# Kernel optimization log

Hardware: AMD Instinct MI355X
Metric: run time of the kernel (lower is better)

Reference implementation:

```python
import jax, jax.numpy as jnp
import numpy as np
from jax import lax

D_MODEL = 64      # feature_dim
D_STATE = 16      # state_dim
D_CONV = 4        # conv_dim
EXPAND = 2
D_INNER = EXPAND * D_MODEL          # 128
DT_RANK = (D_MODEL + 15) // 16      # ceil(d_model/16) = 4, mamba default
IN_DIM = 64
LN_EPS = 1e-3                        # keras LayerNormalization default epsilon


def setup_inputs() -> dict:
    key = jax.random.key(0)
    ks = jax.random.split(key, 12)
    B, L = 16, 8192
    s = 0.02
    x = jax.random.normal(ks[0], (B, L, IN_DIM), jnp.float32)
    W_in = jax.random.normal(ks[1], (IN_DIM, D_MODEL), jnp.float32) * s
    b_in = jnp.zeros((D_MODEL,), jnp.float32)
    in_proj_w = jax.random.normal(ks[2], (D_MODEL, 2 * D_INNER), jnp.float32) * s
    conv_w = jax.random.normal(ks[3], (D_INNER, D_CONV), jnp.float32) * 0.1
    conv_b = jnp.zeros((D_INNER,), jnp.float32)
    x_proj_w = jax.random.normal(ks[4], (D_INNER, DT_RANK + 2 * D_STATE), jnp.float32) * s
    dt_proj_w = jax.random.normal(ks[5], (DT_RANK, D_INNER), jnp.float32) * (DT_RANK ** -0.5)
    # dt bias init so softplus(dt) lands roughly in [dt_min, dt_max]
    dt = jnp.exp(jax.random.uniform(ks[6], (D_INNER,)) * (np.log(0.1) - np.log(0.001)) + np.log(0.001))
    dt_proj_b = dt + jnp.log(-jnp.expm1(-dt))  # inverse softplus
    A_log = jnp.log(jnp.broadcast_to(jnp.arange(1, D_STATE + 1, dtype=jnp.float32), (D_INNER, D_STATE)))
    D_skip = jnp.ones((D_INNER,), jnp.float32)
    out_proj_w = jax.random.normal(ks[7], (D_INNER, D_MODEL), jnp.float32) * s
    ln_gamma = jnp.ones((D_MODEL,), jnp.float32)
    ln_beta = jnp.zeros((D_MODEL,), jnp.float32)
    return {"x": x, "W_in": W_in, "b_in": b_in, "in_proj_w": in_proj_w,
            "conv_w": conv_w, "conv_b": conv_b, "x_proj_w": x_proj_w,
            "dt_proj_w": dt_proj_w, "dt_proj_b": dt_proj_b, "A_log": A_log,
            "D_skip": D_skip, "out_proj_w": out_proj_w,
            "ln_gamma": ln_gamma, "ln_beta": ln_beta}


def reference(x, W_in, b_in, in_proj_w, conv_w, conv_b, x_proj_w,
              dt_proj_w, dt_proj_b, A_log, D_skip, out_proj_w, ln_gamma, ln_beta):
    B, L, _ = x.shape
    # Conv1D kernel_size=1 input projection
    xin = x @ W_in + b_in                          # [B,L,D_MODEL]
    # --- Mamba ---
    xz = xin @ in_proj_w                           # [B,L,2*D_INNER]
    xc, z = xz[..., :D_INNER], xz[..., D_INNER:]
    # causal depthwise conv (groups=d_inner, padding=d_conv-1, crop to L)
    xp = jnp.pad(xc, ((0, 0), (D_CONV - 1, 0), (0, 0)))
    xconv = conv_b
    for k in range(D_CONV):
        xconv = xconv + xp[:, k:k + L, :] * conv_w[:, k]
    u = jax.nn.silu(xconv)                         # [B,L,D_INNER]
    dbc = u @ x_proj_w                             # [B,L,DT_RANK+2*D_STATE]
    dt = jax.nn.softplus(dbc[..., :DT_RANK] @ dt_proj_w + dt_proj_b)   # [B,L,D_INNER]
    Bm = dbc[..., DT_RANK:DT_RANK + D_STATE]       # [B,L,D_STATE]
    Cm = dbc[..., DT_RANK + D_STATE:]              # [B,L,D_STATE]
    A = -jnp.exp(A_log)                            # [D_INNER,D_STATE]

    def step(h, xs):
        dt_t, b_t, c_t, u_t = xs                   # [B,Di],[B,Ds],[B,Ds],[B,Di]
        dA = jnp.exp(dt_t[:, :, None] * A)         # [B,Di,Ds]
        h = dA * h + (dt_t * u_t)[:, :, None] * b_t[:, None, :]
        y = jnp.einsum('bds,bs->bd', h, c_t)
        return h, y

    xs = (jnp.swapaxes(dt, 0, 1), jnp.swapaxes(Bm, 0, 1),
          jnp.swapaxes(Cm, 0, 1), jnp.swapaxes(u, 0, 1))
    h0 = jnp.zeros((B, D_INNER, D_STATE), x.dtype)
    _, ys = lax.scan(step, h0, xs)                 # ys: [L,B,D_INNER]
    y = jnp.swapaxes(ys, 0, 1) + u * D_skip
    y = y * jax.nn.silu(z)
    h_out = y @ out_proj_w                         # [B,L,D_MODEL]
    # residual + LayerNorm
    res = h_out + xin
    mu = jnp.mean(res, axis=-1, keepdims=True)
    var = jnp.mean(jnp.square(res - mu), axis=-1, keepdims=True)
    return ln_gamma * (res - mu) * lax.rsqrt(var + LN_EPS) + ln_beta
```

## Files before the change

kernel.cpp:

```cpp
#include <hip/hip_runtime.h>
#include <hip/hip_bf16.h>
#include <hip/hip_fp16.h>

#define B_SZ   16
#define L_SZ   8192
#define DM     64
#define DI     128
#define NCH    256
#define CLEN   32
#define CH     64
#define RT     80
#define PA     72
#define PU     136
#define PC     132
#define LN_EPS 1e-3f

typedef float  f4 __attribute__((ext_vector_type(4)));
typedef short  s8 __attribute__((ext_vector_type(8)));
typedef unsigned short u16;
typedef unsigned int   u32;
#define MFMA16 __builtin_amdgcn_mfma_f32_16x16x32_bf16

__device__ __forceinline__ u16 f2bfu(float f) {
    u32 u = __float_as_uint(f);
    return (u16)((u + 0x7FFFu + ((u >> 16) & 1u)) >> 16);
}
__device__ __forceinline__ u32 pk2bf(float a, float b) {
    return (u32)f2bfu(a) | ((u32)f2bfu(b) << 16);
}
__device__ __forceinline__ float bflo(u32 u) { return __uint_as_float(u << 16); }
__device__ __forceinline__ float bfhi(u32 u) { return __uint_as_float(u & 0xFFFF0000u); }
__device__ __forceinline__ float bfu2f(u16 h) { return __uint_as_float((u32)h << 16); }
__device__ __forceinline__ float h2f(u32 lo16) {
    return __half2float(__ushort_as_half((u16)(lo16 & 0xFFFFu)));
}
__device__ __forceinline__ float fsig(float v) {
    return __builtin_amdgcn_rcpf(1.f + __expf(-v));
}
__device__ __forceinline__ float fsp(float v) {
    return fmaxf(v, 0.f) + __logf(1.f + __expf(-fabsf(v)));
}

__global__ __launch_bounds__(256) void k_prep(
    const float* __restrict__ W_in, const float* __restrict__ in_proj,
    const float* __restrict__ x_proj, const float* __restrict__ Wout,
    u16* __restrict__ Wf1, u16* __restrict__ Wf2,
    u16* __restrict__ Wf3, u16* __restrict__ Wf4)
{
    const int tid = threadIdx.x;
    for (int g = tid; g < 512; g += 256) {
        int lane = g & 63, ks = (g >> 6) & 1, nt = g >> 7;
        int n = nt * 16 + (lane & 15), kb = ks * 32 + (lane >> 4) * 8;
        for (int j = 0; j < 8; j++) Wf1[g * 8 + j] = f2bfu(W_in[(kb + j) * 64 + n]);
    }
    for (int g = tid; g < 2048; g += 256) {
        int lane = g & 63, ks = (g >> 6) & 1, nt = g >> 7;
        int n = nt * 16 + (lane & 15), kb = ks * 32 + (lane >> 4) * 8;
        for (int j = 0; j < 8; j++) Wf2[g * 8 + j] = f2bfu(in_proj[(kb + j) * 256 + n]);
    }
    for (int g = tid; g < 768; g += 256) {
        int lane = g & 63, ks = (g >> 6) & 3, nt = g >> 8;
        int n = nt * 16 + (lane & 15), kb = ks * 32 + (lane >> 4) * 8;
        for (int j = 0; j < 8; j++)
            Wf3[g * 8 + j] = f2bfu(n < 36 ? x_proj[(kb + j) * 36 + n] : 0.f);
    }
    for (int g = tid; g < 1024; g += 256) {
        int lane = g & 63, ks = (g >> 6) & 3, nt = g >> 8;
        int n = nt * 16 + (lane & 15), kb = ks * 32 + (lane >> 4) * 8;
        for (int j = 0; j < 8; j++) Wf4[g * 8 + j] = f2bfu(Wout[(kb + j) * 64 + n]);
    }
}

__global__ __launch_bounds__(256, 4) void k_frontend(
    const float* __restrict__ x, const float* __restrict__ b_in,
    const float* __restrict__ conv_w, const float* __restrict__ conv_b,
    const float* __restrict__ dt_w, const float* __restrict__ dt_b,
    const u16* __restrict__ Wf1, const u16* __restrict__ Wf2, const u16* __restrict__ Wf3,
    const float* __restrict__ A_log,
    float* __restrict__ xin_g, u32* __restrict__ dtu_g,
    float* __restrict__ B_g, float* __restrict__ C_g, u16* __restrict__ sz_g,
    float* __restrict__ hl_ws, float* __restrict__ sdt_ws)
{
    __shared__ __align__(16) char sm[40736];
    u16*   smA   = (u16*)sm;
    u16*   smB   = (u16*)(sm + 11520);
    u16*   smU   = (u16*)sm;
    float* smDtr = (float*)(sm + 17408);
    float* smBf  = (float*)(sm + 18432);
    u16*   smC   = (u16*)(sm + 23040);
    u32*   smDt  = (u32*)(sm + 23040);

    const int tid = threadIdx.x;
    const int w = tid >> 6, lane = tid & 63;
    const int n16 = lane & 15, quad = lane >> 4;
    const int b = blockIdx.y, c0 = blockIdx.x * CH;
    const long long tokbase = (long long)b * L_SZ + c0;

    for (int idx = tid; idx < RT * 16; idx += 256) {
        int r = idx >> 4, c4 = idx & 15;
        int l = c0 - 3 + r;
        float4 v = make_float4(0.f, 0.f, 0.f, 0.f);
        if (r < 67 && l >= 0)
            v = *(const float4*)(x + ((long long)b * L_SZ + l) * 64 + c4 * 4);
        *(uint2*)((char*)smA + r * 144 + c4 * 8) = make_uint2(pk2bf(v.x, v.y), pk2bf(v.z, v.w));
    }
    __syncthreads();

    {
        s8 b0 = *(const s8*)(Wf1 + ((w * 2 + 0) * 64 + lane) * 8);
        s8 b1 = *(const s8*)(Wf1 + ((w * 2 + 1) * 64 + lane) * 8);
        float bias = b_in[w * 16 + n16];
        for (int m = 0; m < 5; m++) {
            int ar = m * 16 + n16;
            s8 a0 = *(const s8*)(smA + ar * PA + quad * 8);
            s8 a1 = *(const s8*)(smA + ar * PA + 32 + quad * 8);
            f4 acc = {0.f, 0.f, 0.f, 0.f};
            acc = MFMA16(a0, b0, acc, 0, 0, 0);
            acc = MFMA16(a1, b1, acc, 0, 0, 0);
#pragma unroll
            for (int reg = 0; reg < 4; reg++) {
                int rr = m * 16 + quad * 4 + reg;
                float v = acc[reg] + bias;
                smB[rr * PA + w * 16 + n16] = f2bfu(v);
                if (rr >= 3 && rr < 67)
                    xin_g[(tokbase + rr - 3) * 64 + w * 16 + n16] = v;
            }
        }
    }
    __syncthreads();

    {
        s8 bf[4][2];
#pragma unroll
        for (int i = 0; i < 4; i++)
#pragma unroll
            for (int ks = 0; ks < 2; ks++)
                bf[i][ks] = *(const s8*)(Wf2 + (((w * 4 + i) * 2 + ks) * 64 + lane) * 8);
        for (int m = 0; m < 5; m++) {
            int ar = m * 16 + n16;
            s8 a0 = *(const s8*)(smB + ar * PA + quad * 8);
            s8 a1 = *(const s8*)(smB + ar * PA + 32 + quad * 8);
#pragma unroll
            for (int i = 0; i < 4; i++) {
                f4 acc = {0.f, 0.f, 0.f, 0.f};
                acc = MFMA16(a0, bf[i][0], acc, 0, 0, 0);
                acc = MFMA16(a1, bf[i][1], acc, 0, 0, 0);
                int cg = (w * 4 + i) * 16 + n16;
#pragma unroll
                for (int reg = 0; reg < 4; reg++) {
                    int rr = m * 16 + quad * 4 + reg;
                    float v = acc[reg];
                    if (cg < 128) {
                        if (rr < 67) {
                            int l = c0 - 3 + rr;
                            smC[rr * PC + cg] = f2bfu(l >= 0 ? v : 0.f);
                        }
                    } else if (rr >= 3 && rr < 67) {
                        sz_g[(tokbase + rr - 3) * 128 + (cg - 128)] = f2bfu(v * fsig(v));
                    }
                }
            }
        }
    }
    __syncthreads();

    {
        const int d2 = lane * 2, ctb = w * 16;
        float4 cw0 = ((const float4*)conv_w)[d2];
        float4 cw1 = ((const float4*)conv_w)[d2 + 1];
        float cb0 = conv_b[d2], cb1 = conv_b[d2 + 1];
        u32 r0 = *(const u32*)((char*)smC + (ctb + 0) * 264 + lane * 4);
        u32 r1 = *(const u32*)((char*)smC + (ctb + 1) * 264 + lane * 4);
        u32 r2 = *(const u32*)((char*)smC + (ctb + 2) * 264 + lane * 4);
#pragma unroll 4
        for (int j = 0; j < 16; j++) {
            int ct = ctb + j;
            u32 r3 = *(const u32*)((char*)smC + (ct + 3) * 264 + lane * 4);
            float v0 = cb0 + bflo(r0) * cw0.x + bflo(r1) * cw0.y + bflo(r2) * cw0.z + bflo(r3) * cw0.w;
            float v1 = cb1 + bfhi(r0) * cw1.x + bfhi(r1) * cw1.y + bfhi(r2) * cw1.z + bfhi(r3) * cw1.w;
            u32 pk = pk2bf(v0 * fsig(v0), v1 * fsig(v1));
            *(u32*)(smU + ct * PU + d2) = pk;
            r0 = r1; r1 = r2; r2 = r3;
        }
    }
    __syncthreads();

    {
        s8 bf3[3][4];
#pragma unroll
        for (int nt = 0; nt < 3; nt++)
#pragma unroll
            for (int ks = 0; ks < 4; ks++)
                bf3[nt][ks] = *(const s8*)(Wf3 + ((nt * 4 + ks) * 64 + lane) * 8);
        f4 acc[3] = {{0.f,0.f,0.f,0.f},{0.f,0.f,0.f,0.f},{0.f,0.f,0.f,0.f}};
        int ar = w * 16 + n16;
#pragma unroll
        for (int ks = 0; ks < 4; ks++) {
            s8 a = *(const s8*)(smU + ar * PU + ks * 32 + quad * 8);
#pragma unroll
            for (int nt = 0; nt < 3; nt++) acc[nt] = MFMA16(a, bf3[nt][ks], acc[nt], 0, 0, 0);
        }
#pragma unroll
        for (int nt = 0; nt < 3; nt++) {
            int c = nt * 16 + n16;
#pragma unroll
            for (int reg = 0; reg < 4; reg++) {
                int rr = w * 16 + quad * 4 + reg;
                float v = acc[nt][reg];
                long long t = tokbase + rr;
                if (c < 4)       smDtr[rr * 4 + c] = v;
                else if (c < 20) { B_g[t * 16 + (c - 4)] = v; smBf[rr * 16 + (c - 4)] = v; }
                else if (c < 36) C_g[t * 16 + (c - 20)] = v;
            }
        }
    }
    __syncthreads();

    {
        const int o2 = lane * 2, grp = w;
        float w00 = dt_w[o2],       w01 = dt_w[o2 + 1];
        float w10 = dt_w[128 + o2], w11 = dt_w[128 + o2 + 1];
        float w20 = dt_w[256 + o2], w21 = dt_w[256 + o2 + 1];
        float w30 = dt_w[384 + o2], w31 = dt_w[384 + o2 + 1];
        float b0 = dt_b[o2], b1 = dt_b[o2 + 1];
#pragma unroll 4
        for (int j = 0; j < 16; j++) {
            int ct = grp * 16 + j;
            float4 q = *(const float4*)(smDtr + ct * 4);
            float v0 = b0 + q.x * w00 + q.y * w10 + q.z * w20 + q.w * w30;
            float v1 = b1 + q.x * w01 + q.y * w11 + q.z * w21 + q.w * w31;
            u32 hpk = (u32)__half_as_ushort(__float2half_rn(fsp(v0))) |
                      ((u32)__half_as_ushort(__float2half_rn(fsp(v1))) << 16);
            smDt[ct * 64 + lane] = hpk;
            u32 upk = *(const u32*)(smU + ct * PU + o2);
            u32 pk0 = (hpk & 0xFFFFu) | (upk << 16);
            u32 pk1 = (hpk >> 16) | (upk & 0xFFFF0000u);
            *(uint2*)(dtu_g + (tokbase + ct) * 128 + o2) = make_uint2(pk0, pk1);
        }
    }
    __syncthreads();

    {
        const int d = tid & 127, cs = tid >> 7;
        const int j2 = d >> 1, hi = d & 1;
        float A[16];
#pragma unroll
        for (int s = 0; s < 16; s++) A[s] = -__expf(A_log[d * 16 + s]);
        const float A0 = A[0];
        bool chain = true;
#pragma unroll
        for (int s = 1; s < 16; s++)
            chain = chain && (fabsf(A[s] - (float)(s + 1) * A0) <= 1e-4f * fabsf(A[s]));

        float h[16];
#pragma unroll
        for (int s = 0; s < 16; s++) h[s] = 0.f;
        float sdt = 0.f;

        if (chain) {
            for (int i = 0; i < CLEN; i++) {
                int t = cs * CLEN + i;
                u32 q = smDt[t * 64 + j2];
                float dtv = __half2float(__ushort_as_half((u16)(hi ? (q >> 16) : (q & 0xFFFFu))));
                float uv  = bfu2f(smU[t * PU + d]);
                float du  = dtv * uv;  sdt += dtv;
                float4 b0 = *(const float4*)(smBf + t * 16);
                float4 b1 = *(const float4*)(smBf + t * 16 + 4);
                float4 b2 = *(const float4*)(smBf + t * 16 + 8);
                float4 b3 = *(const float4*)(smBf + t * 16 + 12);
                float p  = __expf(dtv * A0);
                float p2 = p * p,  p3 = p2 * p,  p4 = p2 * p2;
                float p8 = p4 * p4;
                h[0]  = p        * h[0]  + du * b0.x;
                h[1]  = p2       * h[1]  + du * b0.y;
                h[2]  = p3       * h[2]  + du * b0.z;
                h[3]  = p4       * h[3]  + du * b0.w;
                h[4]  = (p4*p)   * h[4]  + du * b1.x;
                h[5]  = (p4*p2)  * h[5]  + du * b1.y;
                h[6]  = (p4*p3)  * h[6]  + du * b1.z;
                h[7]  = p8       * h[7]  + du * b1.w;
                h[8]  = (p8*p)   * h[8]  + du * b2.x;
                h[9]  = (p8*p2)  * h[9]  + du * b2.y;
                h[10] = (p8*p3)  * h[10] + du * b2.z;
                h[11] = (p8*p4)  * h[11] + du * b2.w;
                h[12] = (p8*p4*p)  * h[12] + du * b3.x;
                h[13] = (p8*p4*p2) * h[13] + du * b3.y;
                h[14] = (p8*p4*p3) * h[14] + du * b3.z;
                h[15] = (p8*p8)    * h[15] + du * b3.w;
            }
        } else {
            for (int i = 0; i < CLEN; i++) {
                int t = cs * CLEN + i;
                u32 q = smDt[t * 64 + j2];
                float dtv = __half2float(__ushort_as_half((u16)(hi ? (q >> 16) : (q & 0xFFFFu))));
                float uv  = bfu2f(smU[t * PU + d]);
                float du  = dtv * uv;  sdt += dtv;
                const float* Bp = smBf + t * 16;
#pragma unroll
                for (int s = 0; s < 16; s++) h[s] = __expf(dtv * A[s]) * h[s] + du * Bp[s];
            }
        }

        const int ch = blockIdx.x * 2 + cs;
        float4* hp4 = (float4*)(hl_ws + (((long long)b * NCH + ch) * 128 + d) * 16);
        hp4[0] = make_float4(h[0], h[1], h[2], h[3]);
        hp4[1] = make_float4(h[4], h[5], h[6], h[7]);
        hp4[2] = make_float4(h[8], h[9], h[10], h[11]);
        hp4[3] = make_float4(h[12], h[13], h[14], h[15]);
        sdt_ws[((long long)b * NCH + ch) * 128 + d] = sdt;
    }
}

__global__ __launch_bounds__(128) void k_combine(
    const float* __restrict__ A_log, float* __restrict__ hl_ws,
    const float* __restrict__ sdt_ws)
{
    int gid = blockIdx.x * 128 + threadIdx.x;
    int b = gid >> 11;
    int rem = gid & 2047;
    int d = rem >> 4;
    float A = -__expf(A_log[rem]);
    float h = 0.f;
    for (int c = 0; c < NCH; c++) {
        long long o = ((long long)b * NCH + c) * 2048 + rem;
        float v = hl_ws[o];
        float sdt = sdt_ws[((long long)b * NCH + c) * 128 + d];
        hl_ws[o] = h;
        h = __expf(A * sdt) * h + v;
    }
}

__global__ __launch_bounds__(256, 6) void k_backend(
    const u32* __restrict__ dtu_g, const float* __restrict__ B_g,
    const float* __restrict__ C_g, const u16* __restrict__ sz_g,
    const float* __restrict__ A_log, const float* __restrict__ D_skip,
    const float* __restrict__ hin_ws, const float* __restrict__ xin_g,
    const u16* __restrict__ Wf4, const float* __restrict__ gamma,
    const float* __restrict__ beta, float* __restrict__ out)
{
    __shared__ __align__(16) char sm[17408];
    u16*   sy   = (u16*)sm;
    float* smR  = (float*)sm;

    const int tid = threadIdx.x;
    const int cb = blockIdx.x, b = blockIdx.y;
    const long long tok0 = (long long)b * L_SZ + (long long)cb * 64;

    {
        const int d = tid & 127, half = tid >> 7;
        float A[16];
#pragma unroll
        for (int s = 0; s < 16; s++) A[s] = -__expf(A_log[d * 16 + s]);
        const float A0 = A[0];
        bool chain = true;
#pragma unroll
        for (int s = 1; s < 16; s++)
            chain = chain && (fabsf(A[s] - (float)(s + 1) * A0) <= 1e-4f * fabsf(A[s]));

        float h[16];
        {
            const float4* hp = (const float4*)(hin_ws +
                (((long long)b * NCH + 2 * cb + half) * 128 + d) * 16);
            float4 h0 = hp[0], h1 = hp[1], h2 = hp[2], h3 = hp[3];
            h[0]=h0.x; h[1]=h0.y; h[2]=h0.z; h[3]=h0.w;
            h[4]=h1.x; h[5]=h1.y; h[6]=h1.z; h[7]=h1.w;
            h[8]=h2.x; h[9]=h2.y; h[10]=h2.z; h[11]=h2.w;
            h[12]=h3.x; h[13]=h3.y; h[14]=h3.z; h[15]=h3.w;
        }
        const float Dv = D_skip[d];

        if (chain) {
            for (int i = 0; i < CLEN; i++) {
                int t = half * CLEN + i;
                u32 pk = dtu_g[(tok0 + t) * 128 + d];
                float dtv = h2f(pk);
                float uv  = bfhi(pk);
                float du  = dtv * uv;
                const float4* Bp = (const float4*)(B_g + (tok0 + t) * 16);
                float4 b0 = Bp[0], b1 = Bp[1], b2 = Bp[2], b3 = Bp[3];
                const float4* Cp = (const float4*)(C_g + (tok0 + t) * 16);
                float4 c0 = Cp[0], c1 = Cp[1], c2 = Cp[2], c3 = Cp[3];
                float p  = __expf(dtv * A0);
                float p2 = p * p,  p3 = p2 * p,  p4 = p2 * p2;
                float p8 = p4 * p4;
                h[0]  = p        * h[0]  + du * b0.x; float ys = h[0] * c0.x;
                h[1]  = p2       * h[1]  + du * b0.y; ys += h[1]  * c0.y;
                h[2]  = p3       * h[2]  + du * b0.z; ys += h[2]  * c0.z;
                h[3]  = p4       * h[3]  + du * b0.w; ys += h[3]  * c0.w;
                h[4]  = (p4*p)   * h[4]  + du * b1.x; ys += h[4]  * c1.x;
                h[5]  = (p4*p2)  * h[5]  + du * b1.y; ys += h[5]  * c1.y;
                h[6]  = (p4*p3)  * h[6]  + du * b1.z; ys += h[6]  * c1.z;
                h[7]  = p8       * h[7]  + du * b1.w; ys += h[7]  * c1.w;
                h[8]  = (p8*p)   * h[8]  + du * b2.x; ys += h[8]  * c2.x;
                h[9]  = (p8*p2)  * h[9]  + du * b2.y; ys += h[9]  * c2.y;
                h[10] = (p8*p3)  * h[10] + du * b2.z; ys += h[10] * c2.z;
                h[11] = (p8*p4)  * h[11] + du * b2.w; ys += h[11] * c2.w;
                h[12] = (p8*p4*p)  * h[12] + du * b3.x; ys += h[12] * c3.x;
                h[13] = (p8*p4*p2) * h[13] + du * b3.y; ys += h[13] * c3.y;
                h[14] = (p8*p4*p3) * h[14] + du * b3.z; ys += h[14] * c3.z;
                h[15] = (p8*p8)    * h[15] + du * b3.w; ys += h[15] * c3.w;
                float szv = bfu2f(sz_g[(tok0 + t) * 128 + d]);
                sy[t * PU + d] = f2bfu((ys + uv * Dv) * szv);
            }
        } else {
            for (int i = 0; i < CLEN; i++) {
                int t = half * CLEN + i;
                u32 pk = dtu_g[(tok0 + t) * 128 + d];
                float dtv = h2f(pk);
                float uv  = bfhi(pk);
                float du  = dtv * uv;
                const float4* Bp = (const float4*)(B_g + (tok0 + t) * 16);
                float4 b0 = Bp[0], b1 = Bp[1], b2 = Bp[2], b3 = Bp[3];
                float Bv[16] = { b0.x, b0.y, b0.z, b0.w, b1.x, b1.y, b1.z, b1.w,
                                 b2.x, b2.y, b2.z, b2.w, b3.x, b3.y, b3.z, b3.w };
                const float4* Cp = (const float4*)(C_g + (tok0 + t) * 16);
                float4 c0 = Cp[0], c1 = Cp[1], c2 = Cp[2], c3 = Cp[3];
                float Cv[16] = { c0.x, c0.y, c0.z, c0.w, c1.x, c1.y, c1.z, c1.w,
                                 c2.x, c2.y, c2.z, c2.w, c3.x, c3.y, c3.z, c3.w };
                float ys = 0.f;
#pragma unroll
                for (int s = 0; s < 16; s++) {
                    h[s] = __expf(dtv * A[s]) * h[s] + du * Bv[s];
                    ys += h[s] * Cv[s];
                }
                float szv = bfu2f(sz_g[(tok0 + t) * 128 + d]);
                sy[t * PU + d] = f2bfu((ys + uv * Dv) * szv);
            }
        }
    }
    __syncthreads();

    const int w = tid >> 6, lane = tid & 63;
    const int n16 = lane & 15, quad = lane >> 4;
    f4 accm[4];
    {
        s8 bf[4];
#pragma unroll
        for (int ks = 0; ks < 4; ks++)
            bf[ks] = *(const s8*)(Wf4 + ((w * 4 + ks) * 64 + lane) * 8);
#pragma unroll
        for (int m = 0; m < 4; m++) {
            int ar = m * 16 + n16;
            f4 acc = {0.f, 0.f, 0.f, 0.f};
#pragma unroll
            for (int ks = 0; ks < 4; ks++) {
                s8 a = *(const s8*)(sy + ar * PU + ks * 32 + quad * 8);
                acc = MFMA16(a, bf[ks], acc, 0, 0, 0);
            }
            accm[m] = acc;
        }
    }
    __syncthreads();

    {
#pragma unroll
        for (int m = 0; m < 4; m++)
#pragma unroll
            for (int reg = 0; reg < 4; reg++) {
                int rr = m * 16 + quad * 4 + reg;
                smR[rr * 65 + w * 16 + n16] = accm[m][reg];
            }
    }
    __syncthreads();

    {
        int o = tid & 63, wv = tid >> 6;
        float g = gamma[o], bb = beta[o];
        for (int j = 0; j < 16; j++) {
            int rr = wv * 16 + j;
            float r = smR[rr * 65 + o] + xin_g[(tok0 + rr) * 64 + o];
            float s = r;
#pragma unroll
            for (int mS = 0; mS < 6; mS++) s += __shfl_xor(s, 1 << mS, 64);
            float mu = s * (1.f / 64.f);
            float dv = r - mu;
            float vs = dv * dv;
#pragma unroll
            for (int mS = 0; mS < 6; mS++) vs += __shfl_xor(vs, 1 << mS, 64);
            out[(tok0 + rr) * 64 + o] = g * dv * rsqrtf(vs * (1.f / 64.f) + LN_EPS) + bb;
        }
    }
}

extern "C" void kernel_launch(void* const* d_in, const int* in_sizes, int n_in,
                              void* d_out, int out_size, void* d_ws, size_t ws_size,
                              hipStream_t stream)
{
    const float* x       = (const float*)d_in[0];
    const float* W_in    = (const float*)d_in[1];
    const float* b_in    = (const float*)d_in[2];
    const float* in_proj = (const float*)d_in[3];
    const float* conv_w  = (const float*)d_in[4];
    const float* conv_b  = (const float*)d_in[5];
    const float* x_proj  = (const float*)d_in[6];
    const float* dt_w    = (const float*)d_in[7];
    const float* dt_b    = (const float*)d_in[8];
    const float* A_log   = (const float*)d_in[9];
    const float* D_skip  = (const float*)d_in[10];
    const float* Wout    = (const float*)d_in[11];
    const float* gamma   = (const float*)d_in[12];
    const float* beta    = (const float*)d_in[13];
    float* out = (float*)d_out;

    const long long NT = (long long)B_SZ * L_SZ;
    char* ws = (char*)d_ws;
    float*  xin_g = (float*)ws;   ws += NT * 64 * 4;
    u32*    dtu_g = (u32*)ws;     ws += NT * 128 * 4;
    float*  B_g   = (float*)ws;   ws += NT * 16 * 4;
    float*  C_g   = (float*)ws;   ws += NT * 16 * 4;
    u16*    sz_g  = (u16*)ws;     ws += NT * 128 * 2;
    float*  hl_ws  = (float*)ws;  ws += (long long)B_SZ * NCH * 2048 * 4;
    float*  sdt_ws = (float*)ws;  ws += (long long)B_SZ * NCH * 128 * 4;
    u16* Wf1 = (u16*)ws; ws += 4096 * 2;
    u16* Wf2 = (u16*)ws; ws += 16384 * 2;
    u16* Wf3 = (u16*)ws; ws += 6144 * 2;
    u16* Wf4 = (u16*)ws; ws += 8192 * 2;

    k_prep<<<1, 256, 0, stream>>>(W_in, in_proj, x_proj, Wout, Wf1, Wf2, Wf3, Wf4);

    k_frontend<<<dim3(L_SZ / CH, B_SZ), 256, 0, stream>>>(
        x, b_in, conv_w, conv_b, dt_w, dt_b, Wf1, Wf2, Wf3, A_log,
        xin_g, dtu_g, B_g, C_g, sz_g, hl_ws, sdt_ws);

    k_combine<<<256, 128, 0, stream>>>(A_log, hl_ws, sdt_ws);

    k_backend<<<dim3(L_SZ / 64, B_SZ), 256, 0, stream>>>(
        dtu_g, B_g, C_g, sz_g, A_log, D_skip, hl_ws, xin_g,
        Wf4, gamma, beta, out);
}
```

Baseline: 296.0 us.

## Parallelize chunk-state combine with two-level segmented scan across threads

The combine kernel previously ran one thread per (batch, state element), walking all 256 chunks sequentially with only 256 blocks of 128 threads. It now assigns one block per (batch, d) and splits the chunks into 16 segments of 16, scanning each segment locally and then combining segment carries through shared memory. This exposes 16x more parallelism and shortens the serial dependency chain. In exchange it adds extra exp evaluations and uses less coalesced access, since each block touches 16 contiguous floats per chunk row.

```diff
diff --git a/kernel.cpp b/kernel.cpp
--- a/kernel.cpp
+++ b/kernel.cpp
@@ -311,23 +311,42 @@
     }
 }
 
-__global__ __launch_bounds__(128) void k_combine(
+__global__ __launch_bounds__(256) void k_combine(
     const float* __restrict__ A_log, float* __restrict__ hl_ws,
     const float* __restrict__ sdt_ws)
 {
-    int gid = blockIdx.x * 128 + threadIdx.x;
-    int b = gid >> 11;
-    int rem = gid & 2047;
-    int d = rem >> 4;
-    float A = -__expf(A_log[rem]);
-    float h = 0.f;
-    for (int c = 0; c < NCH; c++) {
-        long long o = ((long long)b * NCH + c) * 2048 + rem;
-        float v = hl_ws[o];
-        float sdt = sdt_ws[((long long)b * NCH + c) * 128 + d];
-        hl_ws[o] = h;
+    __shared__ float sH[16 * 16];
+    __shared__ float sCT[16];
+    const int tid = threadIdx.x;
+    const int s = tid & 15, seg = tid >> 4;
+    const int bd = blockIdx.x;
+    const int b = bd >> 7, d = bd & 127;
+    const float A = -__expf(A_log[d * 16 + s]);
+
+    const long long base  = ((long long)b * NCH + seg * 16) * 2048 + d * 16 + s;
+    const long long sbase = ((long long)b * NCH + seg * 16) * 128 + d;
+
+    float hinL[16], cum[16];
+    float h = 0.f, csum = 0.f;
+#pragma unroll
+    for (int j = 0; j < 16; j++) {
+        float v   = hl_ws[base + (long long)j * 2048];
+        float sdt = sdt_ws[sbase + j * 128];
+        hinL[j] = h;  cum[j] = csum;
         h = __expf(A * sdt) * h + v;
-    }
+        csum += sdt;
+    }
+    sH[seg * 16 + s] = h;
+    if (s == 0) sCT[seg] = csum;
+    __syncthreads();
+
+    float hseg = 0.f;
+    for (int k = 0; k < seg; k++)
+        hseg = __expf(A * sCT[k]) * hseg + sH[k * 16 + s];
+
+#pragma unroll
+    for (int j = 0; j < 16; j++)
+        hl_ws[base + (long long)j * 2048] = hinL[j] + __expf(A * cum[j]) * hseg;
 }
 
 __global__ __launch_bounds__(256, 6) void k_backend(
@@ -522,7 +541,7 @@
         x, b_in, conv_w, conv_b, dt_w, dt_b, Wf1, Wf2, Wf3, A_log,
         xin_g, dtu_g, B_g, C_g, sz_g, hl_ws, sdt_ws);
 
-    k_combine<<<256, 128, 0, stream>>>(A_log, hl_ws, sdt_ws);
+    k_combine<<<B_SZ * 128, 256, 0, stream>>>(A_log, hl_ws, sdt_ws);
 
     k_backend<<<dim3(L_SZ / 64, B_SZ), 256, 0, stream>>>(
         dtu_g, B_g, C_g, sz_g, A_log, D_skip, hl_ws, xin_g,
```

After: 295.2 us. No clear change (-0.3%).
